# Optimization experiments

Measured on AMD Instinct MI355X. Metric: run time of the kernel, lower is better.

The kernel has to match this reference:

```python
import jax, jax.numpy as jnp
import numpy as np

DECAY = 0.1  # decay_rate from init

def setup_inputs() -> dict:
    key = jax.random.key(0)
    ks = jax.random.split(key, 6)
    B, S, D, H = 64, 512, 256, 512
    x = jax.random.normal(ks[0], (B, S, D), dtype=jnp.float32)
    # layer 0: Linear(D+H, 4H); layer 1: Linear(H+H, 4H). Stored as [in, out].
    W0 = jax.random.normal(ks[1], (D + H, 4 * H), dtype=jnp.float32) * (1.0 / np.sqrt(D + H))
    b0 = jnp.zeros((4 * H,), dtype=jnp.float32)
    W1 = jax.random.normal(ks[2], (H + H, 4 * H), dtype=jnp.float32) * (1.0 / np.sqrt(H + H))
    b1 = jnp.zeros((4 * H,), dtype=jnp.float32)
    efw = jnp.zeros((1, 1, D), dtype=jnp.float32)  # nn.Parameter(torch.ones) would be ones; use small init via zeros->exp=1 equiv scale
    efw = jnp.ones((1, 1, D), dtype=jnp.float32)
    return {"x": x, "W0": W0, "b0": b0, "W1": W1, "b1": b1, "efw": efw}

def _cell(x_t, h_prev, c_prev, W, b):
    # combined: [B, in+H]; gates: [B, 4H] split into i,f,g,o along feature dim
    gates = jnp.concatenate([x_t, h_prev], axis=1) @ W + b
    i, f, g, o = jnp.split(gates, 4, axis=1)
    i = jax.nn.sigmoid(i)
    f = jax.nn.sigmoid(f + c_prev) * (1.0 - DECAY)  # custom decayed forget gate
    g = jnp.tanh(g)
    o = jax.nn.sigmoid(o)
    c_next = f * c_prev + i * g
    h_next = o * jnp.tanh(c_next)
    return h_next, c_next

def reference(x, W0, b0, W1, b1, efw):
    B, S, D = x.shape
    H = W0.shape[1] // 4
    x = x * jnp.exp(efw)  # elementwise feature weighting
    xs = jnp.transpose(x, (1, 0, 2))  # [S, B, D] for scan over time
    init = (jnp.zeros((B, H), x.dtype), jnp.zeros((B, H), x.dtype),
            jnp.zeros((B, H), x.dtype), jnp.zeros((B, H), x.dtype))

    def step(carry, x_t):
        h0, c0, h1, c1 = carry
        h0, c0 = _cell(x_t, h0, c0, W0, b0)
        h1, c1 = _cell(h0, h1, c1, W1, b1)
        return (h0, c0, h1, c1), h1

    _, ys = jax.lax.scan(step, init, xs)  # ys: [S, B, H]
    return jnp.transpose(ys, (1, 0, 2))  # [B, S, H]
```

## Files before the change

### kernel.cpp

```cpp
#include <hip/hip_runtime.h>
#include <math.h>

#define B_   64
#define S_   512
#define D_   256
#define H_   512
#define G4   2048
#define K0   768
#define K1   1024
#define NWG  256
#define NAH  128
#define NTHR 256
#define BH   32768
#define NROT 4

#define OFF_SCL  192
#define OFF_FLG  512
#define OFF_EPO  4608
#define OFF_TKT  4736
#define OFF_XCN  5120
#define OFF_PFL  5248
#define OFF_H0   9344
#define OFF_H1   (OFF_H0 + 2*BH)
#define OFF_C0   (OFF_H1 + 2*BH)
#define OFF_C1   (OFF_C0 + BH)
#define OFF_ZEND (OFF_C1 + BH)
#define OFF_XBUF OFF_ZEND
#define XBUF_SZ  (8 * NROT * 2 * BH)
#define OFF_END  (OFF_XBUF + XBUF_SZ)

typedef __attribute__((ext_vector_type(4))) float f32x4;
typedef __attribute__((ext_vector_type(8))) short s16x8;
typedef __attribute__((ext_vector_type(4))) short s16x4;

__device__ __forceinline__ float sigm(float v){ return 1.0f/(1.0f+expf(-v)); }
__device__ __forceinline__ unsigned short f2bf(float f){
  unsigned u = __builtin_bit_cast(unsigned, f);
  return (unsigned short)((u + 0x7FFFu + ((u>>16)&1u)) >> 16);
}
__device__ __forceinline__ float bf2f(unsigned short s){
  return __builtin_bit_cast(float, ((unsigned)s) << 16);
}
__device__ __forceinline__ void split8(const float* v, s16x8& h, s16x8& l){
#pragma unroll
  for (int e = 0; e < 8; ++e){
    unsigned short hs = f2bf(v[e]);
    h[e] = (short)hs;
    l[e] = (short)f2bf(v[e] - bf2f(hs));
  }
}
__device__ __forceinline__ void split4(const f32x4& v, s16x4& h, s16x4& l){
#pragma unroll
  for (int e = 0; e < 4; ++e){
    unsigned short hs = f2bf(v[e]);
    h[e] = (short)hs;
    l[e] = (short)f2bf(v[e] - bf2f(hs));
  }
}

#define ALD(p)   __hip_atomic_load((p), __ATOMIC_RELAXED, __HIP_MEMORY_SCOPE_AGENT)
#define AST(p,v) __hip_atomic_store((p), (v), __ATOMIC_RELAXED, __HIP_MEMORY_SCOPE_AGENT)

__device__ __forceinline__ void xadd_noret(unsigned* p, unsigned v){
  asm volatile("global_atomic_add %0, %1, off\n\ts_waitcnt vmcnt(0)"
               :: "v"(p), "v"(v) : "memory");
}
__device__ __forceinline__ unsigned xadd_ret0(unsigned* p){
  unsigned r, z = 0u;
  asm volatile("global_atomic_add %0, %1, %2, off sc0\n\ts_waitcnt vmcnt(0)"
               : "=&v"(r) : "v"(p), "v"(z) : "memory");
  return r;
}
__device__ __forceinline__ void hpub_sc1(float* p, float v){
  unsigned b = __builtin_bit_cast(unsigned, v);
  asm volatile("global_atomic_swap %0, %1, off sc1\n\ts_waitcnt vmcnt(0)"
               :: "v"(p), "v"(b) : "memory");
}
__device__ __forceinline__ void ld_pair_sc1(const float* p0, const float* p1,
                                            f32x4& a, f32x4& b){
  asm volatile("global_load_dwordx4 %0, %2, off sc1\n\t"
               "global_load_dwordx4 %1, %3, off sc1\n\t"
               "s_waitcnt vmcnt(0)"
               : "=&v"(a), "=&v"(b) : "v"(p0), "v"(p1) : "memory");
}

__global__ void lstm_init(const float* __restrict__ efw, float* __restrict__ ws){
  int stride = gridDim.x * blockDim.x;
  for (int j = blockIdx.x * blockDim.x + threadIdx.x; j < OFF_ZEND; j += stride){
    float v = 0.0f;
    if (j >= OFF_SCL && j < OFF_SCL + D_) v = expf(efw[j - OFF_SCL]);
    ws[j] = v;
  }
}

__launch_bounds__(NTHR, 1)
__global__ void lstm_persist(const float* __restrict__ x,
                             const float* __restrict__ W0,
                             const float* __restrict__ b0,
                             const float* __restrict__ W1,
                             const float* __restrict__ b1,
                             float* __restrict__ out,
                             float* __restrict__ ws)
{
  __shared__ short wfH[32*64*8];
  __shared__ short wfL[32*64*8];
  __shared__ short afH[16*64*8];
  __shared__ short afL[16*64*8];
  __shared__ float zB[64*17];
  __shared__ float scl[D_];
  __shared__ int   sslot;

  const int  wg  = blockIdx.x;
  const int  tid = threadIdx.x;
  const bool isA = (wg < NAH);
  const int  u0  = (isA ? wg : wg - NAH) * 4;
  const int  KI  = isA ? 24 : 32;
  const int  nch = isA ? 6 : 8;
  const int  lane = tid & 63;
  const int  wv_  = tid >> 6;

  float* h0 = ws + OFF_H0;
  float* h1 = ws + OFF_H1;
  float* cs = ws + (isA ? OFF_C0 : OFF_C1);
  short* XB = (short*)(ws + OFF_XBUF);
  unsigned* epo = (unsigned*)ws + OFF_EPO;
  unsigned* flg = (unsigned*)ws + OFF_FLG;
  unsigned* tkt = (unsigned*)ws + OFF_TKT;
  unsigned* pfl = (unsigned*)ws + OFF_PFL;

  {
    const float* W = isA ? W0 : W1;
    for (int f = tid; f < KI*64; f += NTHR){
      int ki = f >> 6, ln = f & 63;
      int col = ln & 15, g = col >> 2, u2 = col & 3;
      int kb = ki*32 + ((ln >> 4) << 3);
      const float* wp = W + (size_t)kb * G4 + g * H_ + u0 + u2;
      s16x8 hh, ll;
#pragma unroll
      for (int e = 0; e < 8; ++e){
        float w = wp[(size_t)e * G4];
        unsigned short hs = f2bf(w);
        hh[e] = (short)hs;
        ll[e] = (short)f2bf(w - bf2f(hs));
      }
      *(s16x8*)&wfH[(size_t)f * 8] = hh;
      *(s16x8*)&wfL[(size_t)f * 8] = ll;
    }
  }
  for (int i = tid; i < D_; i += NTHR) scl[i] = ws[OFF_SCL + i];

  int xcc, slot, nx = 1;
  {
    xcc = (int)(__builtin_amdgcn_s_getreg(63508) & 7u);
    if (tid == 0)
      sslot = (int)__hip_atomic_fetch_add(tkt + (size_t)xcc*16, 1u,
                 __ATOMIC_RELAXED, __HIP_MEMORY_SCOPE_AGENT);
    __syncthreads();
    slot = sslot;
  }
  unsigned* xcnt = (unsigned*)ws + OFF_XCN + (size_t)xcc*16;

  auto gbar = [&](unsigned tgt){
    __syncthreads();
    if (tid == 0) AST(flg + (size_t)wg * 16, tgt);
    if (wg == 0 && tid < 64){
      for (;;){
        unsigned m0 = ALD(flg + (size_t)(tid       ) * 16);
        unsigned m1 = ALD(flg + (size_t)(tid +  64) * 16);
        unsigned m2 = ALD(flg + (size_t)(tid + 128) * 16);
        unsigned m3 = ALD(flg + (size_t)(tid + 192) * 16);
        if (__all(m0 >= tgt && m1 >= tgt && m2 >= tgt && m3 >= tgt)) break;
      }
      if (tid == 0){
#pragma unroll
        for (int kq = 0; kq < 8; ++kq) AST(epo + (size_t)kq * 16, tgt);
      }
    }
    if (tid < 64){
      while (ALD(epo + (size_t)(wg & 7) * 16) < tgt)
        __builtin_amdgcn_s_sleep(4);
    }
    __syncthreads();
  };

  auto xbar = [&](unsigned ev){
    __syncthreads();
    if (tid == 0){
      xadd_noret(xcnt, 1u);
      const unsigned tgt = ev * (unsigned)nx;
      while (xadd_ret0(xcnt) < tgt) __builtin_amdgcn_s_sleep(2);
    }
    __syncthreads();
  };

  gbar(1u);
  nx = (int)ALD(tkt + (size_t)xcc * 16);

  const int srow = tid >> 2, sc4 = (tid & 3) << 2;
  auto stage_round = [&](int q, int rot, unsigned tag){
    short* sbw = XB + ((size_t)(xcc * NROT + rot)) * (4 * (size_t)BH);
    for (int g = slot; g < 32; g += nx){
      int fidx = (lane < 4) ? (4*g + lane)
               : (lane < 8 ? 128 + 4*g + (lane - 4) : -1);
      unsigned v = tag;
      for (;;){
        if (fidx >= 0) v = ALD(pfl + (size_t)fidx * 16);
        if (__all(v >= tag)) break;
        __builtin_amdgcn_s_sleep(1);
      }
      const int col = 16*g + sc4;
      const float* g0 = ws + OFF_H0 + (size_t)q * BH + (size_t)srow * H_ + col;
      const float* g1 = ws + OFF_H1 + (size_t)q * BH + (size_t)srow * H_ + col;
      f32x4 a, b; ld_pair_sc1(g0, g1, a, b);
      s16x4 h0h, h0l, h1h, h1l;
      split4(a, h0h, h0l); split4(b, h1h, h1l);
      size_t o = (size_t)srow * H_ + col;
      *(s16x4*)(sbw + o)                  = h0h;
      *(s16x4*)(sbw + (size_t)BH + o)     = h1h;
      *(s16x4*)(sbw + 2*(size_t)BH + o)   = h0l;
      *(s16x4*)(sbw + 3*(size_t)BH + o)   = h1l;
    }
  };

  stage_round(1, 3, 0u);
  xbar(1u);

  const int row_r = tid & 63;
  const int uu    = tid >> 6;
  float bias[4];
  {
    const float* bv = isA ? b0 : b1;
#pragma unroll
    for (int g = 0; g < 4; ++g) bias[g] = bv[g * H_ + u0 + uu];
  }
  __syncthreads();

  const short* sb = nullptr;
  s16x8 rh[4], rl[4];
  const int r16 = tid & 15, ksl = (tid >> 4) & 3, kiq = tid >> 6;

  auto loadregs = [&](int c, int t){
    const int kk = c * 128 + kiq * 32 + ksl * 8;
#pragma unroll
    for (int j = 0; j < 4; ++j){
      const int row = 16 * j + r16;
      if (isA && kk < 256){
        const float* xp = x + ((size_t)row * S_ + t) * D_ + kk;
        float4 v0 = *(const float4*)xp;
        float4 v1 = *(const float4*)(xp + 4);
        float4 s0 = *(const float4*)&scl[kk];
        float4 s1 = *(const float4*)&scl[kk + 4];
        float v[8] = {v0.x*s0.x, v0.y*s0.y, v0.z*s0.z, v0.w*s0.w,
                      v1.x*s1.x, v1.y*s1.y, v1.z*s1.z, v1.w*s1.w};
        split8(v, rh[j], rl[j]);
      } else {
        const short* hp;
        if (isA)           hp = sb + (size_t)row * H_ + (kk - 256);
        else if (kk < 512) hp = sb + (size_t)row * H_ + kk;
        else               hp = sb + BH + (size_t)row * H_ + (kk - 512);
        rh[j] = *(const s16x8*)hp;
        rl[j] = *(const s16x8*)(hp + 2 * BH);
      }
    }
  };

  for (int r = 0; r <= S_; ++r){
    const bool act = isA ? (r < S_) : (r >= 1);
    if (act){
      const int t = isA ? r : r - 1;
      sb = XB + ((size_t)(xcc * NROT + ((r + 3) & 3))) * (4 * (size_t)BH);
      f32x4 aHH = {0.f,0.f,0.f,0.f}, aHL = aHH, aLH = aHH;
      loadregs(0, t);

      for (int c = 0; c < nch; ++c){
        __syncthreads();
#pragma unroll
        for (int j = 0; j < 4; ++j){
          int fs = ((j * 4 + kiq) * 64 + lane) * 8;
          *(s16x8*)&afH[fs] = rh[j];
          *(s16x8*)&afL[fs] = rl[j];
        }
        if (c + 1 < nch) loadregs(c + 1, t);
        __syncthreads();
#pragma unroll
        for (int ki = 0; ki < 4; ++ki){
          int as  = ((wv_ * 4 + ki) * 64 + lane) * 8;
          int wsl = ((c * 4 + ki) * 64 + lane) * 8;
          s16x8 ah = *(const s16x8*)&afH[as];
          s16x8 al = *(const s16x8*)&afL[as];
          s16x8 wh = *(const s16x8*)&wfH[wsl];
          s16x8 wl = *(const s16x8*)&wfL[wsl];
          aHH = __builtin_amdgcn_mfma_f32_16x16x32_bf16(ah, wh, aHH, 0, 0, 0);
          aHL = __builtin_amdgcn_mfma_f32_16x16x32_bf16(ah, wl, aHL, 0, 0, 0);
          aLH = __builtin_amdgcn_mfma_f32_16x16x32_bf16(al, wh, aLH, 0, 0, 0);
        }
      }

      f32x4 accs = (aHH + aHL) + aLH;
#pragma unroll
      for (int reg = 0; reg < 4; ++reg){
        int row = 16 * wv_ + ((lane >> 4) << 2) + reg;
        zB[row * 17 + (lane & 15)] = accs[reg];
      }
      __syncthreads();
      {
        float z[4];
#pragma unroll
        for (int g = 0; g < 4; ++g) z[g] = zB[row_r * 17 + g * 4 + uu] + bias[g];
        const int ui = u0 + uu;
        float c_ = cs[(size_t)row_r * H_ + ui];
        float i_ = sigm(z[0]);
        float f_ = sigm(z[1] + c_) * 0.9f;
        float g_ = tanhf(z[2]);
        float o_ = sigm(z[3]);
        float cn = f_ * c_ + i_ * g_;
        float hn = o_ * tanhf(cn);
        cs[(size_t)row_r * H_ + ui] = cn;
        if (!isA) out[((size_t)row_r * S_ + t) * H_ + ui] = hn;
        float* hw = (isA ? h0 : h1) + (size_t)(r & 1) * BH + (size_t)row_r * H_ + ui;
        hpub_sc1(hw, hn);
      }
    }

    if (r < S_){
      __syncthreads();
      if (tid == 0) AST(pfl + (size_t)wg * 16, (unsigned)(r + 2));
      stage_round(r & 1, r & 3, (unsigned)(r + 2));
      xbar((unsigned)(r + 2));
    }
  }
}

extern "C" void kernel_launch(void* const* d_in, const int* in_sizes, int n_in,
                              void* d_out, int out_size, void* d_ws, size_t ws_size,
                              hipStream_t stream){
  const float* x   = (const float*)d_in[0];
  const float* W0  = (const float*)d_in[1];
  const float* b0  = (const float*)d_in[2];
  const float* W1  = (const float*)d_in[3];
  const float* b1  = (const float*)d_in[4];
  const float* efw = (const float*)d_in[5];
  float* out = (float*)d_out;
  float* ws  = (float*)d_ws;

  if (ws_size < (size_t)OFF_END * sizeof(float)) return;

  lstm_init<<<256, 256, 0, stream>>>(efw, ws);
  lstm_persist<<<NWG, NTHR, 0, stream>>>(x, W0, b0, W1, b1, out, ws);
}
```

Baseline: 6.918 ms.

## Double block threads with split-K MFMA waves and double-buffered fragment staging

Raises the persistent kernel's block size from 256 to 512 threads. The eight waves split each chunk's K range into two halves, with partial sums reduced through two zB buffers before the gate math, which runs on the first 256 threads. The A-fragment LDS buffers are double-buffered so each chunk needs one barrier instead of two. Staging of h0/h1 is split across the two thread halves, each wave polling only its own half's flags, and the xbar sleep is shortened. This aims to shorten the serial per-step critical path by spreading MFMA and staging over more waves, at the cost of more registers and LDS per block and an extra reduction.

```diff
diff --git a/kernel.cpp b/kernel.cpp
--- a/kernel.cpp
+++ b/kernel.cpp
@@ -10,7 +10,7 @@
 #define K1   1024
 #define NWG  256
 #define NAH  128
-#define NTHR 256
+#define NTHR 512
 #define BH   32768
 #define NROT 4
 
@@ -76,12 +76,9 @@
   asm volatile("global_atomic_swap %0, %1, off sc1\n\ts_waitcnt vmcnt(0)"
                :: "v"(p), "v"(b) : "memory");
 }
-__device__ __forceinline__ void ld_pair_sc1(const float* p0, const float* p1,
-                                            f32x4& a, f32x4& b){
-  asm volatile("global_load_dwordx4 %0, %2, off sc1\n\t"
-               "global_load_dwordx4 %1, %3, off sc1\n\t"
-               "s_waitcnt vmcnt(0)"
-               : "=&v"(a), "=&v"(b) : "v"(p0), "v"(p1) : "memory");
+__device__ __forceinline__ void ld1x4_sc1(const float* p, f32x4& a){
+  asm volatile("global_load_dwordx4 %0, %1, off sc1\n\ts_waitcnt vmcnt(0)"
+               : "=&v"(a) : "v"(p) : "memory");
 }
 
 __global__ void lstm_init(const float* __restrict__ efw, float* __restrict__ ws){
@@ -104,9 +101,9 @@
 {
   __shared__ short wfH[32*64*8];
   __shared__ short wfL[32*64*8];
-  __shared__ short afH[16*64*8];
-  __shared__ short afL[16*64*8];
-  __shared__ float zB[64*17];
+  __shared__ short afH2[2][16*64*8];
+  __shared__ short afL2[2][16*64*8];
+  __shared__ float zB[2][64*17];
   __shared__ float scl[D_];
   __shared__ int   sslot;
 
@@ -118,6 +115,8 @@
   const int  nch = isA ? 6 : 8;
   const int  lane = tid & 63;
   const int  wv_  = tid >> 6;
+  const int  rb   = wv_ & 3;
+  const int  kh   = wv_ >> 2;
 
   float* h0 = ws + OFF_H0;
   float* h1 = ws + OFF_H1;
@@ -188,7 +187,7 @@
     if (tid == 0){
       xadd_noret(xcnt, 1u);
       const unsigned tgt = ev * (unsigned)nx;
-      while (xadd_ret0(xcnt) < tgt) __builtin_amdgcn_s_sleep(2);
+      while (xadd_ret0(xcnt) < tgt) __builtin_amdgcn_s_sleep(1);
     }
     __syncthreads();
   };
@@ -196,29 +195,26 @@
   gbar(1u);
   nx = (int)ALD(tkt + (size_t)xcc * 16);
 
-  const int srow = tid >> 2, sc4 = (tid & 3) << 2;
   auto stage_round = [&](int q, int rot, unsigned tag){
     short* sbw = XB + ((size_t)(xcc * NROT + rot)) * (4 * (size_t)BH);
+    const int half = kh;
     for (int g = slot; g < 32; g += nx){
-      int fidx = (lane < 4) ? (4*g + lane)
-               : (lane < 8 ? 128 + 4*g + (lane - 4) : -1);
+      int fidx = (lane < 4) ? ((half ? NAH : 0) + 4*g + lane) : -1;
       unsigned v = tag;
       for (;;){
         if (fidx >= 0) v = ALD(pfl + (size_t)fidx * 16);
         if (__all(v >= tag)) break;
         __builtin_amdgcn_s_sleep(1);
       }
-      const int col = 16*g + sc4;
-      const float* g0 = ws + OFF_H0 + (size_t)q * BH + (size_t)srow * H_ + col;
-      const float* g1 = ws + OFF_H1 + (size_t)q * BH + (size_t)srow * H_ + col;
-      f32x4 a, b; ld_pair_sc1(g0, g1, a, b);
-      s16x4 h0h, h0l, h1h, h1l;
-      split4(a, h0h, h0l); split4(b, h1h, h1l);
-      size_t o = (size_t)srow * H_ + col;
-      *(s16x4*)(sbw + o)                  = h0h;
-      *(s16x4*)(sbw + (size_t)BH + o)     = h1h;
-      *(s16x4*)(sbw + 2*(size_t)BH + o)   = h0l;
-      *(s16x4*)(sbw + 3*(size_t)BH + o)   = h1l;
+      const int rw  = rb * 16 + (lane >> 2);
+      const int col = 16*g + (lane & 3) * 4;
+      const float* src = ws + (half ? OFF_H1 : OFF_H0) + (size_t)q * BH
+                       + (size_t)rw * H_ + col;
+      f32x4 a; ld1x4_sc1(src, a);
+      s16x4 hi, lo; split4(a, hi, lo);
+      size_t o = (size_t)rw * H_ + col;
+      *(s16x4*)(sbw + (size_t)half * BH + o)       = hi;
+      *(s16x4*)(sbw + (size_t)(2 + half) * BH + o) = lo;
     }
   };
 
@@ -226,7 +222,7 @@
   xbar(1u);
 
   const int row_r = tid & 63;
-  const int uu    = tid >> 6;
+  const int uu    = (tid >> 6) & 3;
   float bias[4];
   {
     const float* bv = isA ? b0 : b1;
@@ -236,13 +232,15 @@
   __syncthreads();
 
   const short* sb = nullptr;
-  s16x8 rh[4], rl[4];
-  const int r16 = tid & 15, ksl = (tid >> 4) & 3, kiq = tid >> 6;
+  s16x8 rh[2], rl[2];
+  const int r16 = lane & 15, ksl = lane >> 4;
 
   auto loadregs = [&](int c, int t){
-    const int kk = c * 128 + kiq * 32 + ksl * 8;
-#pragma unroll
-    for (int j = 0; j < 4; ++j){
+#pragma unroll
+    for (int jj = 0; jj < 2; ++jj){
+      const int sidx = jj * 8 + wv_;
+      const int j = sidx >> 2, ki = sidx & 3;
+      const int kk = c * 128 + ki * 32 + ksl * 8;
       const int row = 16 * j + r16;
       if (isA && kk < 256){
         const float* xp = x + ((size_t)row * S_ + t) * D_ + kk;
@@ -252,15 +250,23 @@
         float4 s1 = *(const float4*)&scl[kk + 4];
         float v[8] = {v0.x*s0.x, v0.y*s0.y, v0.z*s0.z, v0.w*s0.w,
                       v1.x*s1.x, v1.y*s1.y, v1.z*s1.z, v1.w*s1.w};
-        split8(v, rh[j], rl[j]);
+        split8(v, rh[jj], rl[jj]);
       } else {
         const short* hp;
         if (isA)           hp = sb + (size_t)row * H_ + (kk - 256);
         else if (kk < 512) hp = sb + (size_t)row * H_ + kk;
         else               hp = sb + BH + (size_t)row * H_ + (kk - 512);
-        rh[j] = *(const s16x8*)hp;
-        rl[j] = *(const s16x8*)(hp + 2 * BH);
-      }
+        rh[jj] = *(const s16x8*)hp;
+        rl[jj] = *(const s16x8*)(hp + 2 * BH);
+      }
+    }
+  };
+  auto writefrags = [&](int b){
+#pragma unroll
+    for (int jj = 0; jj < 2; ++jj){
+      const int fs = ((jj * 8 + wv_) * 64 + lane) * 8;
+      *(s16x8*)&afH2[b][fs] = rh[jj];
+      *(s16x8*)&afL2[b][fs] = rl[jj];
     }
   };
 
@@ -268,26 +274,23 @@
     const bool act = isA ? (r < S_) : (r >= 1);
     if (act){
       const int t = isA ? r : r - 1;
-      sb = XB + ((size_t)(xcc * NROT + ((r + 3) & 3))) * (4 * (size_t)BH);
+      sb = (const short*)(XB + ((size_t)(xcc * NROT + ((r + 3) & 3))) * (4 * (size_t)BH));
       f32x4 aHH = {0.f,0.f,0.f,0.f}, aHL = aHH, aLH = aHH;
       loadregs(0, t);
+      writefrags(0);
 
       for (int c = 0; c < nch; ++c){
         __syncthreads();
-#pragma unroll
-        for (int j = 0; j < 4; ++j){
-          int fs = ((j * 4 + kiq) * 64 + lane) * 8;
-          *(s16x8*)&afH[fs] = rh[j];
-          *(s16x8*)&afL[fs] = rl[j];
-        }
-        if (c + 1 < nch) loadregs(c + 1, t);
-        __syncthreads();
-#pragma unroll
-        for (int ki = 0; ki < 4; ++ki){
-          int as  = ((wv_ * 4 + ki) * 64 + lane) * 8;
+        if (c + 1 < nch){ loadregs(c + 1, t); writefrags((c + 1) & 1); }
+        const short* aH = afH2[c & 1];
+        const short* aL = afL2[c & 1];
+#pragma unroll
+        for (int ki2 = 0; ki2 < 2; ++ki2){
+          const int ki = kh * 2 + ki2;
+          int as  = ((rb * 4 + ki) * 64 + lane) * 8;
           int wsl = ((c * 4 + ki) * 64 + lane) * 8;
-          s16x8 ah = *(const s16x8*)&afH[as];
-          s16x8 al = *(const s16x8*)&afL[as];
+          s16x8 ah = *(const s16x8*)&aH[as];
+          s16x8 al = *(const s16x8*)&aL[as];
           s16x8 wh = *(const s16x8*)&wfH[wsl];
           s16x8 wl = *(const s16x8*)&wfL[wsl];
           aHH = __builtin_amdgcn_mfma_f32_16x16x32_bf16(ah, wh, aHH, 0, 0, 0);
@@ -299,14 +302,16 @@
       f32x4 accs = (aHH + aHL) + aLH;
 #pragma unroll
       for (int reg = 0; reg < 4; ++reg){
-        int row = 16 * wv_ + ((lane >> 4) << 2) + reg;
-        zB[row * 17 + (lane & 15)] = accs[reg];
+        int row = 16 * rb + ((lane >> 4) << 2) + reg;
+        zB[kh][row * 17 + (lane & 15)] = accs[reg];
       }
       __syncthreads();
-      {
+      if (tid < 256){
         float z[4];
 #pragma unroll
-        for (int g = 0; g < 4; ++g) z[g] = zB[row_r * 17 + g * 4 + uu] + bias[g];
+        for (int g = 0; g < 4; ++g)
+          z[g] = zB[0][row_r * 17 + g * 4 + uu]
+               + zB[1][row_r * 17 + g * 4 + uu] + bias[g];
         const int ui = u0 + uu;
         float c_ = cs[(size_t)row_r * H_ + ui];
         float i_ = sigm(z[0]);
```

Measured after the change: 6.962 ms. No clear change (+0.6%).
